# Kernel optimization log

Hardware: AMD Instinct MI355X
Metric: run time of the kernel (lower is better)

The kernel has to match this reference:

```python
import jax, jax.numpy as jnp
import numpy as np

HIDDEN = 1024
NUM_HEADS = 16
HEAD_DIM = HIDDEN // NUM_HEADS  # 64
WINDOW = 33
PAD = WINDOW // 2
B, S = 2, 2048


def setup_inputs() -> dict:
    key = jax.random.key(0)
    k = jax.random.split(key, 5)
    x = jax.random.normal(k[0], (B, S, HIDDEN), dtype=jnp.float32)
    w_qkv = jax.random.normal(k[1], (3 * HIDDEN, HIDDEN), dtype=jnp.float32) * 0.02
    b_qkv = jax.random.normal(k[2], (3 * HIDDEN,), dtype=jnp.float32) * 0.02
    w_out = jax.random.normal(k[3], (HIDDEN, HIDDEN), dtype=jnp.float32) * 0.02
    b_out = jax.random.normal(k[4], (HIDDEN,), dtype=jnp.float32) * 0.02
    return {"x": x, "w_qkv": w_qkv, "b_qkv": b_qkv, "w_out": w_out, "b_out": b_out}


def reference(x, w_qkv, b_qkv, w_out, b_out):
    b, s, _ = x.shape
    # fused qkv projection: (B,S,3H)
    qkv = x @ w_qkv.T + b_qkv
    # (B, NH, S, 3*HD) then split into q,k,v -- matches torch reshape+chunk layout
    qkv = qkv.reshape(b, s, NUM_HEADS, 3 * HEAD_DIM).transpose(0, 2, 1, 3)
    q, k, v = jnp.split(qkv, 3, axis=-1)  # each (B, NH, S, HD)
    # zero-pad keys/values along sequence; NOTE: original does NOT mask the
    # padded positions -- zero keys yield score 0 and participate in softmax.
    k_pad = jnp.pad(k, ((0, 0), (0, 0), (PAD, PAD), (0, 0)))
    v_pad = jnp.pad(v, ((0, 0), (0, 0), (PAD, PAD), (0, 0)))
    # window gather indices: position i attends padded slots i..i+WINDOW-1
    idx = jnp.arange(s)[:, None] + jnp.arange(WINDOW)[None, :]  # (S, W)
    k_win = k_pad[:, :, idx, :]  # (B, NH, S, W, HD)
    v_win = v_pad[:, :, idx, :]  # (B, NH, S, W, HD)
    scores = jnp.einsum("bhsd,bhswd->bhsw", q, k_win) / jnp.sqrt(
        jnp.asarray(HEAD_DIM, dtype=q.dtype)
    )
    attn = jax.nn.softmax(scores, axis=-1)
    ctx = jnp.einsum("bhsw,bhswd->bhsd", attn, v_win)  # (B, NH, S, HD)
    ctx = ctx.transpose(0, 2, 1, 3).reshape(b, s, HIDDEN)
    return ctx @ w_out.T + b_out
```

## Files before the change

### kernel.cpp

```cpp
#include <hip/hip_runtime.h>
#include <stdint.h>

#define NHEADS 16
#define HDIM 64
#define WIN 33
#define BATCH 2
#define SEQ 2048
#define MROWS (BATCH*SEQ)
#define PARTSZ (BATCH*NHEADS*SEQ*HDIM)

using f32x4 = __attribute__((ext_vector_type(4))) float;
using bf16x8 = __attribute__((ext_vector_type(8))) short;

__device__ inline short f2bf(float f) {
    union { float f; uint32_t u; } c; c.f = f;
    uint32_t u = c.u;
    uint32_t r = (u + 0x7fffu + ((u >> 16) & 1u)) >> 16;
    return (short)(uint16_t)r;
}

#define GLL16(g, l) __builtin_amdgcn_global_load_lds( \
        (const __attribute__((address_space(1))) void*)(g), \
        (__attribute__((address_space(3))) void*)(l), 16, 0, 0)
#define WAITV(n)  asm volatile("s_waitcnt vmcnt(" #n ")" ::: "memory")
#define WAITL0()  asm volatile("s_waitcnt lgkmcnt(0)" ::: "memory")
#define SBAR()    __builtin_amdgcn_s_barrier()
#define SCHED0()  __builtin_amdgcn_sched_barrier(0)

__global__ __launch_bounds__(256)
void cvt3_k(const float* __restrict__ x,  short* __restrict__ xb,
            const float* __restrict__ w1, short* __restrict__ w1b,
            const float* __restrict__ w2, short* __restrict__ w2b)
{
    const int i = blockIdx.x * 256 + threadIdx.x;
    const float* src; short* dstp; int off;
    if (i < 524288)      { src = x;  dstp = xb;  off = i; }
    else if (i < 917504) { src = w1; dstp = w1b; off = i - 524288; }
    else                 { src = w2; dstp = w2b; off = i - 917504; }
    const f32x4 v0 = *(const f32x4*)(src + (size_t)off * 8);
    const f32x4 v1 = *(const f32x4*)(src + (size_t)off * 8 + 4);
    bf16x8 o;
    o[0] = f2bf(v0[0]); o[1] = f2bf(v0[1]); o[2] = f2bf(v0[2]); o[3] = f2bf(v0[3]);
    o[4] = f2bf(v1[0]); o[5] = f2bf(v1[1]); o[6] = f2bf(v1[2]); o[7] = f2bf(v1[3]);
    *(bf16x8*)(dstp + (size_t)off * 8) = o;
}

__global__ __launch_bounds__(512, 4)
void gemm1_k(const short* __restrict__ A, const short* __restrict__ Bm,
             const float* __restrict__ bias, short* __restrict__ dst)
{
    __shared__ short As[2][8192];
    __shared__ short Bs[2][12288];
    const int tid  = threadIdx.x;
    const int lane = tid & 63;
    const int wv   = tid >> 6;
    const int wr = wv >> 2, wc = wv & 3;
    const int q15 = lane & 15, p = lane >> 4;

    int bid = blockIdx.x;
    bid = (bid & 7) * 64 + (bid >> 3);
    const int tmi = bid & 31, tni = bid >> 5;
    const int tm = tmi << 7;
    const int tn = tni * 192;

    const int ssl = (tid & 7) ^ ((tid >> 4) & 7);
    const short* Ag = A  + (size_t)(tm + (tid >> 3)) * 1024 + ssl * 8;
    const short* Bg = Bm + (size_t)(tn + (tid >> 3)) * 1024 + ssl * 8;

#define STGA(d, rowoff, koff) GLL16(Ag + (size_t)(rowoff) * 1024 + (koff), &As[d][(rowoff) * 64 + tid * 8])
#define STGB(d, rowoff, koff) GLL16(Bg + (size_t)(rowoff) * 1024 + (koff), &Bs[d][(rowoff) * 64 + tid * 8])
#define STAGE_AB(d, koff) do { STGA(d,0,koff); STGA(d,64,koff); \
                               STGB(d,0,koff); STGB(d,64,koff); STGB(d,128,koff); } while (0)

    f32x4 acc[4][3];
#pragma unroll
    for (int mi = 0; mi < 4; ++mi)
#pragma unroll
        for (int ni = 0; ni < 3; ++ni) acc[mi][ni] = (f32x4)0.f;

    const int swz  = q15 >> 1;
    const int arow = (wr * 64 + q15) * 64;
    const int brow = (wc * 48 + q15) * 64;
    const int s0o  = (p ^ swz) * 8;
    const int s1o  = ((4 + p) ^ swz) * 8;

    STAGE_AB(0, 0);
    STAGE_AB(1, 64);
    WAITV(5); SBAR(); SCHED0();

#pragma unroll
    for (int kt = 0; kt < 16; ++kt) {
        const int par = kt & 1;
        const short* asd = &As[par][0];
        const short* bsd = &Bs[par][0];
        bf16x8 af[4][2], bf[3][2];

#pragma unroll
        for (int mi = 0; mi < 4; ++mi) {
            af[mi][0] = *(const bf16x8*)(asd + arow + mi * 1024 + s0o);
            af[mi][1] = *(const bf16x8*)(asd + arow + mi * 1024 + s1o);
        }
#pragma unroll
        for (int ni = 0; ni < 3; ++ni) {
            bf[ni][0] = *(const bf16x8*)(bsd + brow + ni * 1024 + s0o);
            bf[ni][1] = *(const bf16x8*)(bsd + brow + ni * 1024 + s1o);
        }
        WAITL0(); SBAR(); SCHED0();

        if (kt < 14) STAGE_AB(par, (kt + 2) * 64);
        __builtin_amdgcn_s_setprio(1);
#pragma unroll
        for (int mi = 0; mi < 4; ++mi)
#pragma unroll
            for (int ni = 0; ni < 3; ++ni) {
                acc[mi][ni] = __builtin_amdgcn_mfma_f32_16x16x32_bf16(af[mi][0], bf[ni][0], acc[mi][ni], 0, 0, 0);
                acc[mi][ni] = __builtin_amdgcn_mfma_f32_16x16x32_bf16(af[mi][1], bf[ni][1], acc[mi][ni], 0, 0, 0);
            }
        __builtin_amdgcn_s_setprio(0);
        SCHED0();
        if (kt < 14)       { WAITV(5); SBAR(); SCHED0(); }
        else if (kt == 14) { WAITV(0); SBAR(); SCHED0(); }
    }
#undef STGA
#undef STGB
#undef STAGE_AB

#pragma unroll
    for (int mi = 0; mi < 4; ++mi) {
#pragma unroll
        for (int ni = 0; ni < 3; ++ni) {
            const int c    = wc * 48 + ni * 16 + q15;
            const int part = c >> 6;
            const int dd   = c & 63;
            const int row0 = tm + wr * 64 + mi * 16 + p * 4;
            const float bv = bias[tn + c];
            const size_t pbase = (size_t)part * PARTSZ;
#pragma unroll
            for (int r = 0; r < 4; ++r) {
                const int row = row0 + r;
                const int b   = row >> 11;
                const int s   = row & 2047;
                const size_t hb = pbase + ((((size_t)b << 4) + tni) << 17);
                const size_t addr = (part == 2)
                    ? hb + ((size_t)dd << 11) + s
                    : hb + ((size_t)s << 6) + dd;
                dst[addr] = f2bf(acc[mi][ni][r] + bv);
            }
        }
    }
}

__global__ __launch_bounds__(256, 3)
void gemm2_k(const short* __restrict__ A, const short* __restrict__ Bm,
             const float* __restrict__ bias, float* __restrict__ C)
{
    __shared__ short As[3][2048];
    __shared__ short Bs[3][4096];
    const int tid  = threadIdx.x;
    const int lane = tid & 63;
    const int wc   = tid >> 6;
    const int q15 = lane & 15, p = lane >> 4;

    int bid = blockIdx.x;
    bid = (bid & 7) * 64 + (bid >> 3);
    const int tm = (bid & 63) << 6;
    const int tn = (bid >> 6) << 7;

    const int rb  = tid >> 2;
    const int ssl = (tid & 3) ^ ((rb >> 1) & 3);
    const short* Ag = A  + (size_t)(tm + rb) * 1024 + ssl * 8;
    const short* Bg = Bm + (size_t)(tn + rb) * 1024 + ssl * 8;

#define STAGE2(tt, db) do {                                  \
        const int _ko = (tt) * 32;                           \
        GLL16(Ag + _ko,         &As[db][tid * 8]);           \
        GLL16(Bg + _ko,         &Bs[db][tid * 8]);           \
        GLL16(Bg + _ko + 65536, &Bs[db][2048 + tid * 8]);    \
    } while (0)

    f32x4 acc[4][2];
#pragma unroll
    for (int mi = 0; mi < 4; ++mi)
#pragma unroll
        for (int ni = 0; ni < 2; ++ni) acc[mi][ni] = (f32x4)0.f;

    int oA[4], oB[2];
#pragma unroll
    for (int mi = 0; mi < 4; ++mi) {
        const int row = mi * 16 + q15;
        oA[mi] = row * 32 + (p ^ ((row >> 1) & 3)) * 8;
    }
#pragma unroll
    for (int ni = 0; ni < 2; ++ni) {
        const int row = wc * 32 + ni * 16 + q15;
        oB[ni] = row * 32 + (p ^ ((row >> 1) & 3)) * 8;
    }

    STAGE2(0, 0); STAGE2(1, 1);
    WAITV(3); SBAR(); SCHED0();

    for (int t = 0; t < 32; ++t) {
        const int cb = t % 3;
        if (t < 30) STAGE2(t + 2, (t + 2) % 3);
        bf16x8 af[4], bfr[2];
#pragma unroll
        for (int mi = 0; mi < 4; ++mi) af[mi] = *(const bf16x8*)(&As[cb][oA[mi]]);
#pragma unroll
        for (int ni = 0; ni < 2; ++ni) bfr[ni] = *(const bf16x8*)(&Bs[cb][oB[ni]]);
        __builtin_amdgcn_s_setprio(1);
#pragma unroll
        for (int mi = 0; mi < 4; ++mi)
#pragma unroll
            for (int ni = 0; ni < 2; ++ni)
                acc[mi][ni] = __builtin_amdgcn_mfma_f32_16x16x32_bf16(af[mi], bfr[ni], acc[mi][ni], 0, 0, 0);
        __builtin_amdgcn_s_setprio(0);
        SCHED0();
        if (t < 30)       { WAITV(3); SBAR(); SCHED0(); }
        else if (t == 30) { WAITV(0); SBAR(); SCHED0(); }
    }
#undef STAGE2

#pragma unroll
    for (int mi = 0; mi < 4; ++mi) {
#pragma unroll
        for (int ni = 0; ni < 2; ++ni) {
            const int col  = tn + wc * 32 + ni * 16 + q15;
            const int row0 = tm + mi * 16 + p * 4;
            const float bv = bias[col];
#pragma unroll
            for (int r = 0; r < 4; ++r)
                C[(size_t)(row0 + r) * 1024 + col] = acc[mi][ni][r] + bv;
        }
    }
}

__global__ __launch_bounds__(256)
void swattn4_k(const short* __restrict__ qkvb, short* __restrict__ ctx)
{
    __shared__ short Ks[96 * 64];
    __shared__ short Vt[64 * 104];
    const int tid  = threadIdx.x;
    const int lane = tid & 63;
    const int w    = tid >> 6;
    const int q15  = lane & 15;
    const int p    = lane >> 4;
    const int tile = blockIdx.x & 31;
    const int bh   = blockIdx.x >> 5;
    const int b    = bh >> 4, h = bh & 15;
    const int s0   = tile * 64;
    const short* qbase  = qkvb + ((size_t)bh << 17);
    const short* kbase  = qbase + PARTSZ;
    const short* vtbase = qbase + 2 * PARTSZ;

#pragma unroll
    for (int c = 0; c < 3; ++c) {
        const int idx = c * 256 + tid;
        const int row = idx >> 3;
        const int sli = idx & 7;
        const int pos = s0 - 16 + row;
        bf16x8 kv = (bf16x8)0;
        if (pos >= 0 && pos < SEQ)
            kv = *(const bf16x8*)(kbase + (size_t)pos * 64 + sli * 8);
        *(bf16x8*)(Ks + row * 64 + ((sli ^ (row & 7)) << 3)) = kv;
    }
#pragma unroll
    for (int c = 0; c < 4; ++c) {
        const int idx = c * 256 + tid;
        const int d   = idx >> 4;
        const int sli = idx & 15;
        if (sli < 12) {
            const int pos = s0 - 16 + sli * 8;
            bf16x8 vv = (bf16x8)0;
            if (pos >= 0 && pos <= SEQ - 8)
                vv = *(const bf16x8*)(vtbase + (size_t)d * SEQ + pos);
            *(bf16x8*)(Vt + d * 104 + sli * 8) = vv;
        }
    }
    __syncthreads();

    const int qrow = s0 + w * 16 + q15;
    const bf16x8 qf0 = *(const bf16x8*)(qbase + (size_t)qrow * 64 + p * 8);
    const bf16x8 qf1 = *(const bf16x8*)(qbase + (size_t)qrow * 64 + 32 + p * 8);

    f32x4 accs[6];
#pragma unroll
    for (int t = 0; t < 6; ++t) accs[t] = (f32x4)0.f;
#pragma unroll
    for (int t = 0; t < 6; ++t) {
        const int row = t * 16 + q15;
        const int sw  = row & 7;
        const bf16x8 kf0 = *(const bf16x8*)(Ks + row * 64 + ((p ^ sw) << 3));
        const bf16x8 kf1 = *(const bf16x8*)(Ks + row * 64 + (((p + 4) ^ sw) << 3));
        accs[t] = __builtin_amdgcn_mfma_f32_16x16x32_bf16(kf0, qf0, accs[t], 0, 0, 0);
        accs[t] = __builtin_amdgcn_mfma_f32_16x16x32_bf16(kf1, qf1, accs[t], 0, 0, 0);
    }

    const int qloc = w * 16 + q15;
    float m = -1e30f;
#pragma unroll
    for (int t = 0; t < 6; ++t)
#pragma unroll
        for (int r = 0; r < 4; ++r) {
            const int n = t * 16 + p * 4 + r;
            const bool valid = (n >= qloc) && (n <= qloc + 32);
            const float v = valid ? accs[t][r] * 0.125f : -1e30f;
            accs[t][r] = v;
            m = fmaxf(m, v);
        }
    m = fmaxf(m, __shfl_xor(m, 16));
    m = fmaxf(m, __shfl_xor(m, 32));
    float sum = 0.f;
#pragma unroll
    for (int t = 0; t < 6; ++t)
#pragma unroll
        for (int r = 0; r < 4; ++r) {
            const float e = __expf(accs[t][r] - m);
            accs[t][r] = e;
            sum += e;
        }
    sum += __shfl_xor(sum, 16);
    sum += __shfl_xor(sum, 32);
    const float inv = 1.f / sum;

    uint32_t pk[6][2];
#pragma unroll
    for (int t = 0; t < 6; ++t)
#pragma unroll
        for (int rp = 0; rp < 2; ++rp) {
            const float lo = accs[t][2 * rp] * inv;
            const float hi = accs[t][2 * rp + 1] * inv;
            uint32_t o;
            asm("v_cvt_pk_bf16_f32 %0, %1, %2" : "=v"(o) : "v"(lo), "v"(hi));
            pk[t][rp] = o;
        }
    uint32_t afu[3][4];
#pragma unroll
    for (int t = 0; t < 6; ++t)
#pragma unroll
        for (int rp = 0; rp < 2; ++rp)
#pragma unroll
            for (int bb = 0; bb < 2; ++bb) {
                const int src = q15 + (((2 * p + bb) & 3) << 4);
                const uint32_t v = __shfl((int)pk[t][rp], src);
                if ((t & 1) == (p >> 1))
                    afu[t >> 1][2 * bb + rp] = v;
            }
    union U { uint32_t u[4]; bf16x8 v; };
    U u0, u1, u2;
#pragma unroll
    for (int f = 0; f < 4; ++f) { u0.u[f] = afu[0][f]; u1.u[f] = afu[1][f]; u2.u[f] = afu[2][f]; }
    const bf16x8 af0 = u0.v, af1 = u1.v, af2 = u2.v;

    f32x4 accp[4];
#pragma unroll
    for (int dt = 0; dt < 4; ++dt) accp[dt] = (f32x4)0.f;
#pragma unroll
    for (int dt = 0; dt < 4; ++dt) {
        const short* vr = Vt + (dt * 16 + q15) * 104 + p * 8;
        const bf16x8 vf0 = *(const bf16x8*)(vr);
        const bf16x8 vf1 = *(const bf16x8*)(vr + 32);
        const bf16x8 vf2 = *(const bf16x8*)(vr + 64);
        accp[dt] = __builtin_amdgcn_mfma_f32_16x16x32_bf16(af0, vf0, accp[dt], 0, 0, 0);
        accp[dt] = __builtin_amdgcn_mfma_f32_16x16x32_bf16(af1, vf1, accp[dt], 0, 0, 0);
        accp[dt] = __builtin_amdgcn_mfma_f32_16x16x32_bf16(af2, vf2, accp[dt], 0, 0, 0);
    }

#pragma unroll
    for (int dt = 0; dt < 4; ++dt) {
        const int d = dt * 16 + q15;
#pragma unroll
        for (int r = 0; r < 4; ++r) {
            const int s = s0 + w * 16 + p * 4 + r;
            ctx[(((size_t)(b * SEQ + s)) << 10) + h * 64 + d] = f2bf(accp[dt][r]);
        }
    }
}

extern "C" void kernel_launch(void* const* d_in, const int* in_sizes, int n_in,
                              void* d_out, int out_size, void* d_ws, size_t ws_size,
                              hipStream_t stream)
{
    const float* x     = (const float*)d_in[0];
    const float* w_qkv = (const float*)d_in[1];
    const float* b_qkv = (const float*)d_in[2];
    const float* w_out = (const float*)d_in[3];
    const float* b_out = (const float*)d_in[4];
    float* out = (float*)d_out;

    char* ws = (char*)d_ws;
    short* x_bf    = (short*)(ws);
    short* wqkv_bf = (short*)(ws + (8ull  << 20));
    short* wout_bf = (short*)(ws + (14ull << 20));
    short* qkvb    = (short*)(ws + (16ull << 20));
    short* ctx     = (short*)(ws + (48ull << 20));

    cvt3_k<<<dim3(4096), 256, 0, stream>>>(x, x_bf, w_qkv, wqkv_bf, w_out, wout_bf);

    gemm1_k<<<dim3(512), 512, 0, stream>>>(x_bf, wqkv_bf, b_qkv, qkvb);

    swattn4_k<<<dim3((SEQ / 64) * BATCH * NHEADS), 256, 0, stream>>>(qkvb, (short*)ctx);

    gemm2_k<<<dim3(512), 256, 0, stream>>>(ctx, wout_bf, b_out, out);
}
```

Before: 77.25 us.

## Restructure output GEMM to double-buffered K=64 tiles with early reuse barrier

The output projection GEMM moves from a triple-buffered K=32 pipeline to a double-buffered K=64 pipeline. Each stage issues six 16-byte LDS-direct loads per thread and runs two MFMAs per accumulator. Fragments are read into registers first, then a barrier lets the next prefetch overwrite the same buffer. This halves the loop iterations and barrier count, and a new 8-way XOR swizzle matches the wider rows. LDS use grows from about 36KB to 48KB per block even though launch bounds now request 4 blocks per CU, so occupancy may not actually rise.

Result: faster. 70.57 us (-8.6%).

```diff
diff --git a/kernel.cpp b/kernel.cpp
--- a/kernel.cpp
+++ b/kernel.cpp
@@ -150,12 +150,12 @@
     }
 }
 
-__global__ __launch_bounds__(256, 3)
+__global__ __launch_bounds__(256, 4)
 void gemm2_k(const short* __restrict__ A, const short* __restrict__ Bm,
              const float* __restrict__ bias, float* __restrict__ C)
 {
-    __shared__ short As[3][2048];
-    __shared__ short Bs[3][4096];
+    __shared__ short As[2][4096];
+    __shared__ short Bs[2][8192];
     const int tid  = threadIdx.x;
     const int lane = tid & 63;
     const int wc   = tid >> 6;
@@ -166,17 +166,15 @@
     const int tm = (bid & 63) << 6;
     const int tn = (bid >> 6) << 7;
 
-    const int rb  = tid >> 2;
-    const int ssl = (tid & 3) ^ ((rb >> 1) & 3);
-    const short* Ag = A  + (size_t)(tm + rb) * 1024 + ssl * 8;
-    const short* Bg = Bm + (size_t)(tn + rb) * 1024 + ssl * 8;
-
-#define STAGE2(tt, db) do {                                  \
-        const int _ko = (tt) * 32;                           \
-        GLL16(Ag + _ko,         &As[db][tid * 8]);           \
-        GLL16(Bg + _ko,         &Bs[db][tid * 8]);           \
-        GLL16(Bg + _ko + 65536, &Bs[db][2048 + tid * 8]);    \
-    } while (0)
+    const int ssl = (tid & 7) ^ ((tid >> 4) & 7);
+    const short* Ag = A  + (size_t)(tm + (tid >> 3)) * 1024 + ssl * 8;
+    const short* Bg = Bm + (size_t)(tn + (tid >> 3)) * 1024 + ssl * 8;
+
+#define STGA2(d, rowoff, koff) GLL16(Ag + (size_t)(rowoff) * 1024 + (koff), &As[d][(rowoff) * 64 + tid * 8])
+#define STGB2(d, rowoff, koff) GLL16(Bg + (size_t)(rowoff) * 1024 + (koff), &Bs[d][(rowoff) * 64 + tid * 8])
+#define STAGE2_AB(d, koff) do { STGA2(d,0,koff); STGA2(d,32,koff); \
+                                STGB2(d,0,koff); STGB2(d,32,koff); \
+                                STGB2(d,64,koff); STGB2(d,96,koff); } while (0)
 
     f32x4 acc[4][2];
 #pragma unroll
@@ -184,41 +182,52 @@
 #pragma unroll
         for (int ni = 0; ni < 2; ++ni) acc[mi][ni] = (f32x4)0.f;
 
-    int oA[4], oB[2];
-#pragma unroll
-    for (int mi = 0; mi < 4; ++mi) {
-        const int row = mi * 16 + q15;
-        oA[mi] = row * 32 + (p ^ ((row >> 1) & 3)) * 8;
-    }
-#pragma unroll
-    for (int ni = 0; ni < 2; ++ni) {
-        const int row = wc * 32 + ni * 16 + q15;
-        oB[ni] = row * 32 + (p ^ ((row >> 1) & 3)) * 8;
-    }
-
-    STAGE2(0, 0); STAGE2(1, 1);
-    WAITV(3); SBAR(); SCHED0();
-
-    for (int t = 0; t < 32; ++t) {
-        const int cb = t % 3;
-        if (t < 30) STAGE2(t + 2, (t + 2) % 3);
-        bf16x8 af[4], bfr[2];
-#pragma unroll
-        for (int mi = 0; mi < 4; ++mi) af[mi] = *(const bf16x8*)(&As[cb][oA[mi]]);
-#pragma unroll
-        for (int ni = 0; ni < 2; ++ni) bfr[ni] = *(const bf16x8*)(&Bs[cb][oB[ni]]);
+    const int swz  = q15 >> 1;
+    const int arow = q15 * 64;
+    const int brow = (wc * 32 + q15) * 64;
+    const int s0o  = (p ^ swz) * 8;
+    const int s1o  = ((4 + p) ^ swz) * 8;
+
+    STAGE2_AB(0, 0);
+    STAGE2_AB(1, 64);
+    WAITV(6); SBAR(); SCHED0();
+
+#pragma unroll
+    for (int kt = 0; kt < 16; ++kt) {
+        const int par = kt & 1;
+        const short* asd = &As[par][0];
+        const short* bsd = &Bs[par][0];
+        bf16x8 af[4][2], bf[2][2];
+
+#pragma unroll
+        for (int mi = 0; mi < 4; ++mi) {
+            af[mi][0] = *(const bf16x8*)(asd + arow + mi * 1024 + s0o);
+            af[mi][1] = *(const bf16x8*)(asd + arow + mi * 1024 + s1o);
+        }
+#pragma unroll
+        for (int ni = 0; ni < 2; ++ni) {
+            bf[ni][0] = *(const bf16x8*)(bsd + brow + ni * 1024 + s0o);
+            bf[ni][1] = *(const bf16x8*)(bsd + brow + ni * 1024 + s1o);
+        }
+        WAITL0(); SBAR(); SCHED0();
+
+        if (kt < 14) STAGE2_AB(par, (kt + 2) * 64);
         __builtin_amdgcn_s_setprio(1);
 #pragma unroll
         for (int mi = 0; mi < 4; ++mi)
 #pragma unroll
-            for (int ni = 0; ni < 2; ++ni)
-                acc[mi][ni] = __builtin_amdgcn_mfma_f32_16x16x32_bf16(af[mi], bfr[ni], acc[mi][ni], 0, 0, 0);
+            for (int ni = 0; ni < 2; ++ni) {
+                acc[mi][ni] = __builtin_amdgcn_mfma_f32_16x16x32_bf16(af[mi][0], bf[ni][0], acc[mi][ni], 0, 0, 0);
+                acc[mi][ni] = __builtin_amdgcn_mfma_f32_16x16x32_bf16(af[mi][1], bf[ni][1], acc[mi][ni], 0, 0, 0);
+            }
         __builtin_amdgcn_s_setprio(0);
         SCHED0();
-        if (t < 30)       { WAITV(3); SBAR(); SCHED0(); }
-        else if (t == 30) { WAITV(0); SBAR(); SCHED0(); }
-    }
-#undef STAGE2
+        if (kt < 14)       { WAITV(6); SBAR(); SCHED0(); }
+        else if (kt == 14) { WAITV(0); SBAR(); SCHED0(); }
+    }
+#undef STGA2
+#undef STGB2
+#undef STAGE2_AB
 
 #pragma unroll
     for (int mi = 0; mi < 4; ++mi) {
```
